# Optimization experiments

Measured on AMD Instinct MI355X. Metric: run time of the kernel, lower is better.

The kernel has to match this reference:

```python
import jax, jax.numpy as jnp
import numpy as np

B, CK, CQ, CV, CO, H, W = 4, 256, 256, 256, 64, 24, 24


def setup_inputs() -> dict:
    key = jax.random.key(0)
    ks = jax.random.split(key, 9)
    s = lambda k, shape, fan: jax.random.normal(k, shape, jnp.float32) * (fan ** -0.5)
    return {
        "key": jax.random.normal(ks[0], (B, CK, H, W), jnp.float32),
        "query": jax.random.normal(ks[1], (B, CQ, H, W), jnp.float32),
        "value": jax.random.normal(ks[2], (B, CV, H, W), jnp.float32),
        "Wk": s(ks[3], (CO, CK), CK),   # 1x1 conv weight for key transform
        "bk": jnp.zeros((CO,), jnp.float32),
        "Wq": s(ks[4], (CO, CQ), CQ),   # 1x1 conv weight for query transform
        "bq": jnp.zeros((CO,), jnp.float32),
        "wf": s(ks[5], (CO,), CO),      # channel-flattening 1x1 conv (CO -> 1)
        "bf": jnp.zeros((), jnp.float32),
    }


def reference(key, query, value, Wk, bk, Wq, bq, wf, bf):
    b, _, hq, wq = query.shape
    nk = key.shape[2] * key.shape[3]
    nq = hq * wq
    # 1x1 conv == per-pixel linear; flatten spatial to (B, N, CO)
    k_ = jnp.einsum('bchw,oc->bhwo', key, Wk).reshape(b, nk, -1) + bk
    q_ = jnp.einsum('bchw,oc->bhwo', query, Wq).reshape(b, nq, -1) + bq
    # broadcast add: (B, Nk, 1, CO) + (B, 1, Nq, CO) -> tanh -> reduce channels
    pre = jnp.tanh(k_[:, :, None, :] + q_[:, None, :, :])
    scores = jnp.einsum('bkqc,c->bkq', pre, wf) + bf
    attn = jax.nn.sigmoid(scores)                      # (B, Nk, Nq)
    v_ = value.reshape(b, value.shape[1], nk)          # (B, CV, Nk)
    out = jnp.einsum('bkq,bck->bcq', attn, v_)         # (B, CV, Nq)
    return out.reshape(b, value.shape[1], hq, wq)
```

## Files before the change

### kernel.cpp

```cpp
#include <hip/hip_runtime.h>
#include <hip/hip_bf16.h>

#define BB 4
#define CIN 256
#define CO 64
#define NN 576
#define NKC 18
#define NQT 36

typedef __attribute__((ext_vector_type(8))) short short8;
typedef __attribute__((ext_vector_type(4))) float floatx4;

__device__ __forceinline__ unsigned short f2bf(float f) {
    unsigned int u = __float_as_uint(f);
    unsigned int r = (u + 0x7fffu + ((u >> 16) & 1u)) >> 16;
    return (unsigned short)r;
}

__global__ void __launch_bounds__(256) prep_kernel(
    const float* __restrict__ key, const float* __restrict__ query,
    const float* __restrict__ value,
    const float* __restrict__ Wk, const float* __restrict__ Wq,
    const float* __restrict__ bk, const float* __restrict__ bq,
    float* __restrict__ ek, float* __restrict__ eq,
    unsigned short* __restrict__ Vp)
{
    __shared__ float red[4][4][64][4];
    __shared__ float ex[16 * 69];

    int bid = blockIdx.x;
    int t = threadIdx.x;
    int l = t & 63;
    int w = __builtin_amdgcn_readfirstlane(t >> 6);

    if (bid < 288) {
        int z  = bid / 144;
        int r  = bid % 144;
        int b  = r / 36;
        int nt = r % 36;
        int n0 = nt * 16;
        const float* x = z ? query : key;
        const float* W = z ? Wq : Wk;

        floatx4 acc[4] = {{0.f,0.f,0.f,0.f},{0.f,0.f,0.f,0.f},
                          {0.f,0.f,0.f,0.f},{0.f,0.f,0.f,0.f}};

        #pragma unroll
        for (int kci = 0; kci < 2; ++kci) {
            int kc = w + kci * 4;
            int cbase = kc * 32 + (l >> 4) * 8;
            const float* xp = x + ((size_t)b * CIN + cbase) * NN + n0 + (l & 15);
            uint4 bu;
            {
                float x0 = xp[0 * NN], x1 = xp[1 * NN], x2 = xp[2 * NN], x3 = xp[3 * NN];
                float x4 = xp[4 * NN], x5 = xp[5 * NN], x6 = xp[6 * NN], x7 = xp[7 * NN];
                bu.x = (unsigned)f2bf(x0) | ((unsigned)f2bf(x1) << 16);
                bu.y = (unsigned)f2bf(x2) | ((unsigned)f2bf(x3) << 16);
                bu.z = (unsigned)f2bf(x4) | ((unsigned)f2bf(x5) << 16);
                bu.w = (unsigned)f2bf(x6) | ((unsigned)f2bf(x7) << 16);
            }
            short8 bx = *(short8*)&bu;
            #pragma unroll
            for (int mt = 0; mt < 4; ++mt) {
                const float4* wp = (const float4*)(W + (size_t)(mt * 16 + (l & 15)) * CIN + cbase);
                float4 w0 = wp[0], w1 = wp[1];
                uint4 au;
                au.x = (unsigned)f2bf(w0.x) | ((unsigned)f2bf(w0.y) << 16);
                au.y = (unsigned)f2bf(w0.z) | ((unsigned)f2bf(w0.w) << 16);
                au.z = (unsigned)f2bf(w1.x) | ((unsigned)f2bf(w1.y) << 16);
                au.w = (unsigned)f2bf(w1.z) | ((unsigned)f2bf(w1.w) << 16);
                acc[mt] = __builtin_amdgcn_mfma_f32_16x16x32_bf16(*(short8*)&au, bx, acc[mt], 0, 0, 0);
            }
        }
        #pragma unroll
        for (int mt = 0; mt < 4; ++mt)
            #pragma unroll
            for (int rr = 0; rr < 4; ++rr)
                red[w][mt][l][rr] = acc[mt][rr];
        __syncthreads();

        const float* bias = z ? bq : bk;
        #pragma unroll
        for (int rr = 0; rr < 4; ++rr) {
            float v = red[0][w][l][rr] + red[1][w][l][rr]
                    + red[2][w][l][rr] + red[3][w][l][rr];
            int o = w * 16 + (l >> 4) * 4 + rr;
            ex[(l & 15) * 69 + o] = __expf(2.0f * (v + bias[o]));
        }
        __syncthreads();

        float* outp = z ? eq : ek;
        float* obase = outp + ((size_t)b * NN + n0) * CO;
        #pragma unroll
        for (int i = 0; i < 4; ++i) {
            int idx = t + i * 256;
            int n = idx >> 6, o = idx & 63;
            obase[(size_t)n * CO + o] = ex[n * 69 + o];
        }
    } else {
        int funit = (bid - 288) * 4 + w;
        int b  = funit / 288;
        int r2 = funit % 288;
        int ct = r2 / NKC;
        int kc = r2 % NKC;
        int c = ct * 16 + (l & 15);
        int k = kc * 32 + (l >> 4) * 8;
        const float4* p = (const float4*)(value + ((size_t)b * CIN + c) * NN + k);
        float4 v0 = p[0], v1 = p[1];
        uint4 u;
        u.x = (unsigned)f2bf(v0.x) | ((unsigned)f2bf(v0.y) << 16);
        u.y = (unsigned)f2bf(v0.z) | ((unsigned)f2bf(v0.w) << 16);
        u.z = (unsigned)f2bf(v1.x) | ((unsigned)f2bf(v1.y) << 16);
        u.w = (unsigned)f2bf(v1.z) | ((unsigned)f2bf(v1.w) << 16);
        *(uint4*)(Vp + (((size_t)b * 16 + ct) * NKC + kc) * 512 + l * 8) = u;
    }
}

__global__ void __launch_bounds__(256, 3) attn_pack_kernel(
    const float* __restrict__ ek, const float* __restrict__ eq,
    const float* __restrict__ wf, const float* __restrict__ bfp,
    unsigned short* __restrict__ Bp)
{
    int b  = blockIdx.z;
    int k0 = blockIdx.y * 32;
    int q0 = blockIdx.x * 64;
    int t  = threadIdx.x;
    int l  = t & 63;
    int w  = __builtin_amdgcn_readfirstlane(t >> 6);

    __shared__ float eqs[64 * 65];
    __shared__ float eks[32 * 68];
    __shared__ float w2s[64];
    __shared__ float Cs;
    __shared__ float sc[32 * 65];

    const float4* esrc = (const float4*)(eq + ((size_t)b * NN + q0) * CO);
    #pragma unroll
    for (int i = 0; i < 4; ++i) {
        int f4 = t + i * 256;
        int row = f4 >> 4, c4 = (f4 & 15) * 4;
        float4 v = esrc[f4];
        int a = row * 65 + c4;
        eqs[a] = v.x; eqs[a + 1] = v.y; eqs[a + 2] = v.z; eqs[a + 3] = v.w;
    }
    const float4* ksrc = (const float4*)(ek + ((size_t)b * NN + k0) * CO);
    #pragma unroll
    for (int i = 0; i < 2; ++i) {
        int f4 = t + i * 256;
        int row = f4 >> 4, c4 = (f4 & 15) * 4;
        *(float4*)&eks[row * 68 + c4] = ksrc[f4];
    }
    if (t < 64) {
        float v = wf[t];
        w2s[t] = 2.0f * v;
        #pragma unroll
        for (int s = 32; s; s >>= 1) v += __shfl_xor(v, s, 64);
        if (t == 0) Cs = v + bfp[0];
    }
    __syncthreads();

    float C = Cs;
    float4 eqv[16];
    #pragma unroll
    for (int i = 0; i < 16; ++i) {
        int a = l * 65 + i * 4;
        eqv[i].x = eqs[a]; eqv[i].y = eqs[a + 1];
        eqv[i].z = eqs[a + 2]; eqv[i].w = eqs[a + 3];
    }

    #pragma unroll 1
    for (int kk = 0; kk < 8; ++kk) {
        int krow = w * 8 + kk;
        const float* ekr = &eks[krow * 68];
        float a0 = 0.f, a1 = 0.f, a2 = 0.f, a3 = 0.f;
        #pragma unroll
        for (int i = 0; i < 16; ++i) {
            float4 k4 = *(const float4*)(ekr + i * 4);
            float4 w4 = *(const float4*)&w2s[i * 4];
            float4 e4 = eqv[i];
            a0 = fmaf(w4.x, __builtin_amdgcn_rcpf(fmaf(k4.x, e4.x, 1.0f)), a0);
            a1 = fmaf(w4.y, __builtin_amdgcn_rcpf(fmaf(k4.y, e4.y, 1.0f)), a1);
            a2 = fmaf(w4.z, __builtin_amdgcn_rcpf(fmaf(k4.z, e4.z, 1.0f)), a2);
            a3 = fmaf(w4.w, __builtin_amdgcn_rcpf(fmaf(k4.w, e4.w, 1.0f)), a3);
        }
        float score = C - (a0 + a1) - (a2 + a3);
        float sg = __builtin_amdgcn_rcpf(1.0f + __expf(-score));
        sc[krow * 65 + l] = sg;
    }
    __syncthreads();

    int col = w * 16 + (l & 15);
    int row = (l >> 4) * 8;
    uint4 o;
    o.x = (unsigned)f2bf(sc[(row + 0) * 65 + col]) | ((unsigned)f2bf(sc[(row + 1) * 65 + col]) << 16);
    o.y = (unsigned)f2bf(sc[(row + 2) * 65 + col]) | ((unsigned)f2bf(sc[(row + 3) * 65 + col]) << 16);
    o.z = (unsigned)f2bf(sc[(row + 4) * 65 + col]) | ((unsigned)f2bf(sc[(row + 5) * 65 + col]) << 16);
    o.w = (unsigned)f2bf(sc[(row + 6) * 65 + col]) | ((unsigned)f2bf(sc[(row + 7) * 65 + col]) << 16);
    size_t qt = (size_t)blockIdx.x * 4 + w;
    *(uint4*)(Bp + (((size_t)b * NQT + qt) * NKC + blockIdx.y) * 512 + l * 8) = o;
}

__global__ void __launch_bounds__(256) av_mfma_kernel(
    const unsigned short* __restrict__ Vp,
    const unsigned short* __restrict__ Bp,
    float* __restrict__ out)
{
    int b  = blockIdx.z;
    int ct = blockIdx.y;
    int qx = blockIdx.x;
    int t  = threadIdx.x;
    int l  = t & 63;
    int w  = __builtin_amdgcn_readfirstlane(t >> 6);

    floatx4 acc[4] = {{0.f,0.f,0.f,0.f},{0.f,0.f,0.f,0.f},
                      {0.f,0.f,0.f,0.f},{0.f,0.f,0.f,0.f}};

    const unsigned short* abase = Vp + ((size_t)b * 16 + ct) * NKC * 512 + l * 8;
    const unsigned short* bbase = Bp + ((size_t)b * NQT + (size_t)qx * 4) * NKC * 512 + l * 8;

    for (int kc = w; kc < NKC; kc += 4) {
        short8 a = *(const short8*)(abase + (size_t)kc * 512);
        #pragma unroll
        for (int qt = 0; qt < 4; ++qt) {
            short8 bq = *(const short8*)(bbase + ((size_t)qt * NKC + kc) * 512);
            acc[qt] = __builtin_amdgcn_mfma_f32_16x16x32_bf16(a, bq, acc[qt], 0, 0, 0);
        }
    }

    __shared__ float red[4][64][17];
    #pragma unroll
    for (int qt = 0; qt < 4; ++qt)
        #pragma unroll
        for (int r = 0; r < 4; ++r)
            red[w][l][qt * 4 + r] = acc[qt][r];
    __syncthreads();

    int q = qx * 64 + w * 16 + (l & 15);
    #pragma unroll
    for (int r = 0; r < 4; ++r) {
        float s = red[0][l][w * 4 + r] + red[1][l][w * 4 + r]
                + red[2][l][w * 4 + r] + red[3][l][w * 4 + r];
        int c = ct * 16 + (l >> 4) * 4 + r;
        out[((size_t)b * CIN + c) * NN + q] = s;
    }
}

extern "C" void kernel_launch(void* const* d_in, const int* in_sizes, int n_in,
                              void* d_out, int out_size, void* d_ws, size_t ws_size,
                              hipStream_t stream) {
    const float* key   = (const float*)d_in[0];
    const float* query = (const float*)d_in[1];
    const float* value = (const float*)d_in[2];
    const float* Wk    = (const float*)d_in[3];
    const float* bk    = (const float*)d_in[4];
    const float* Wq    = (const float*)d_in[5];
    const float* bq    = (const float*)d_in[6];
    const float* wf    = (const float*)d_in[7];
    const float* bf    = (const float*)d_in[8];
    float* out = (float*)d_out;

    float* ws = (float*)d_ws;
    float* ek = ws;
    float* eq = ek + (size_t)BB * NN * CO;
    unsigned short* Vp = (unsigned short*)(eq + (size_t)BB * NN * CO);
    unsigned short* Bp = Vp + (size_t)BB * 16 * NKC * 512;

    prep_kernel<<<576, 256, 0, stream>>>(key, query, value, Wk, Wq, bk, bq, ek, eq, Vp);

    dim3 ga(NN / 64, NN / 32, BB);
    attn_pack_kernel<<<ga, 256, 0, stream>>>(ek, eq, wf, bf, Bp);

    dim3 gm(NN / 64, 16, BB);
    av_mfma_kernel<<<gm, 256, 0, stream>>>(Vp, Bp, out);
}
```

Baseline: 108.1 us.

## Stage input tile in LDS for coalesced loads and fold tanh scale into ek

The projection stage now loads each 256x16 input tile with coalesced float4 reads, transposes it into shared memory, and swaps the MFMA operand roles so the output tile is stored row-contiguous. This replaces the strided per-element global reads of the old path. It also folds the factor 2 on wf into ek by scaling ek by 0.5 and using a 0.5 constant in the reciprocal. That saves a multiply per weight load, and the tanh identity stays mathematically the same. The cost is extra LDS (about 16KB more) and an additional barrier.

```diff
diff --git a/kernel.cpp b/kernel.cpp
--- a/kernel.cpp
+++ b/kernel.cpp
@@ -6,6 +6,7 @@
 #define CO 64
 #define NN 576
 #define NKC 18
+#define NMT 36
 #define NQT 36
 
 typedef __attribute__((ext_vector_type(8))) short short8;
@@ -25,8 +26,9 @@
     float* __restrict__ ek, float* __restrict__ eq,
     unsigned short* __restrict__ Vp)
 {
+    __shared__ float xs[16 * 260];
     __shared__ float red[4][4][64][4];
-    __shared__ float ex[16 * 69];
+    __shared__ float ex[16 * 68];
 
     int bid = blockIdx.x;
     int t = threadIdx.x;
@@ -36,66 +38,77 @@
     if (bid < 288) {
         int z  = bid / 144;
         int r  = bid % 144;
-        int b  = r / 36;
-        int nt = r % 36;
-        int n0 = nt * 16;
+        int b  = r / NMT;
+        int mt = r % NMT;
+        int n0 = mt * 16;
         const float* x = z ? query : key;
         const float* W = z ? Wq : Wk;
 
+        const float* xbase = x + (size_t)b * CIN * NN + n0;
+        #pragma unroll
+        for (int i = 0; i < 4; ++i) {
+            int f4 = t + i * 256;
+            int c = f4 >> 2, nl4 = (f4 & 3) * 4;
+            float4 v = *(const float4*)(xbase + (size_t)c * NN + nl4);
+            xs[(nl4 + 0) * 260 + c] = v.x;
+            xs[(nl4 + 1) * 260 + c] = v.y;
+            xs[(nl4 + 2) * 260 + c] = v.z;
+            xs[(nl4 + 3) * 260 + c] = v.w;
+        }
+        __syncthreads();
+
         floatx4 acc[4] = {{0.f,0.f,0.f,0.f},{0.f,0.f,0.f,0.f},
                           {0.f,0.f,0.f,0.f},{0.f,0.f,0.f,0.f}};
-
         #pragma unroll
         for (int kci = 0; kci < 2; ++kci) {
-            int kc = w + kci * 4;
-            int cbase = kc * 32 + (l >> 4) * 8;
-            const float* xp = x + ((size_t)b * CIN + cbase) * NN + n0 + (l & 15);
-            uint4 bu;
-            {
-                float x0 = xp[0 * NN], x1 = xp[1 * NN], x2 = xp[2 * NN], x3 = xp[3 * NN];
-                float x4 = xp[4 * NN], x5 = xp[5 * NN], x6 = xp[6 * NN], x7 = xp[7 * NN];
-                bu.x = (unsigned)f2bf(x0) | ((unsigned)f2bf(x1) << 16);
-                bu.y = (unsigned)f2bf(x2) | ((unsigned)f2bf(x3) << 16);
-                bu.z = (unsigned)f2bf(x4) | ((unsigned)f2bf(x5) << 16);
-                bu.w = (unsigned)f2bf(x6) | ((unsigned)f2bf(x7) << 16);
+            int kc = w * 2 + kci;
+            int c0 = kc * 32 + (l >> 4) * 8;
+            float4 xa = *(const float4*)&xs[(l & 15) * 260 + c0];
+            float4 xb = *(const float4*)&xs[(l & 15) * 260 + c0 + 4];
+            uint4 au;
+            au.x = (unsigned)f2bf(xa.x) | ((unsigned)f2bf(xa.y) << 16);
+            au.y = (unsigned)f2bf(xa.z) | ((unsigned)f2bf(xa.w) << 16);
+            au.z = (unsigned)f2bf(xb.x) | ((unsigned)f2bf(xb.y) << 16);
+            au.w = (unsigned)f2bf(xb.z) | ((unsigned)f2bf(xb.w) << 16);
+            short8 xf = *(short8*)&au;
+            #pragma unroll
+            for (int nt = 0; nt < 4; ++nt) {
+                const float4* wp = (const float4*)(W + (size_t)(nt * 16 + (l & 15)) * CIN + c0);
+                float4 w0 = wp[0], w1 = wp[1];
+                uint4 bu;
+                bu.x = (unsigned)f2bf(w0.x) | ((unsigned)f2bf(w0.y) << 16);
+                bu.y = (unsigned)f2bf(w0.z) | ((unsigned)f2bf(w0.w) << 16);
+                bu.z = (unsigned)f2bf(w1.x) | ((unsigned)f2bf(w1.y) << 16);
+                bu.w = (unsigned)f2bf(w1.z) | ((unsigned)f2bf(w1.w) << 16);
+                acc[nt] = __builtin_amdgcn_mfma_f32_16x16x32_bf16(xf, *(short8*)&bu, acc[nt], 0, 0, 0);
             }
-            short8 bx = *(short8*)&bu;
-            #pragma unroll
-            for (int mt = 0; mt < 4; ++mt) {
-                const float4* wp = (const float4*)(W + (size_t)(mt * 16 + (l & 15)) * CIN + cbase);
-                float4 w0 = wp[0], w1 = wp[1];
-                uint4 au;
-                au.x = (unsigned)f2bf(w0.x) | ((unsigned)f2bf(w0.y) << 16);
-                au.y = (unsigned)f2bf(w0.z) | ((unsigned)f2bf(w0.w) << 16);
-                au.z = (unsigned)f2bf(w1.x) | ((unsigned)f2bf(w1.y) << 16);
-                au.w = (unsigned)f2bf(w1.z) | ((unsigned)f2bf(w1.w) << 16);
-                acc[mt] = __builtin_amdgcn_mfma_f32_16x16x32_bf16(*(short8*)&au, bx, acc[mt], 0, 0, 0);
-            }
-        }
-        #pragma unroll
-        for (int mt = 0; mt < 4; ++mt)
+        }
+        #pragma unroll
+        for (int nt = 0; nt < 4; ++nt)
             #pragma unroll
             for (int rr = 0; rr < 4; ++rr)
-                red[w][mt][l][rr] = acc[mt][rr];
+                red[w][nt][l][rr] = acc[nt][rr];
         __syncthreads();
 
         const float* bias = z ? bq : bk;
+        float scale = z ? 1.0f : 0.5f;
         #pragma unroll
         for (int rr = 0; rr < 4; ++rr) {
             float v = red[0][w][l][rr] + red[1][w][l][rr]
                     + red[2][w][l][rr] + red[3][w][l][rr];
-            int o = w * 16 + (l >> 4) * 4 + rr;
-            ex[(l & 15) * 69 + o] = __expf(2.0f * (v + bias[o]));
+            int o = w * 16 + (l & 15);
+            int n = (l >> 4) * 4 + rr;
+            ex[n * 68 + o] = scale * __expf(2.0f * (v + bias[o]));
         }
         __syncthreads();
 
-        float* outp = z ? eq : ek;
+        float* outp  = z ? eq : ek;
         float* obase = outp + ((size_t)b * NN + n0) * CO;
         #pragma unroll
         for (int i = 0; i < 4; ++i) {
             int idx = t + i * 256;
             int n = idx >> 6, o = idx & 63;
-            obase[(size_t)n * CO + o] = ex[n * 69 + o];
+            obase[idx] = ex[n * 68 + o];
         }
     } else {
         int funit = (bid - 288) * 4 + w;
@@ -152,7 +165,7 @@
     }
     if (t < 64) {
         float v = wf[t];
-        w2s[t] = 2.0f * v;
+        w2s[t] = v;
         #pragma unroll
         for (int s = 32; s; s >>= 1) v += __shfl_xor(v, s, 64);
         if (t == 0) Cs = v + bfp[0];
@@ -178,10 +191,10 @@
             float4 k4 = *(const float4*)(ekr + i * 4);
             float4 w4 = *(const float4*)&w2s[i * 4];
             float4 e4 = eqv[i];
-            a0 = fmaf(w4.x, __builtin_amdgcn_rcpf(fmaf(k4.x, e4.x, 1.0f)), a0);
-            a1 = fmaf(w4.y, __builtin_amdgcn_rcpf(fmaf(k4.y, e4.y, 1.0f)), a1);
-            a2 = fmaf(w4.z, __builtin_amdgcn_rcpf(fmaf(k4.z, e4.z, 1.0f)), a2);
-            a3 = fmaf(w4.w, __builtin_amdgcn_rcpf(fmaf(k4.w, e4.w, 1.0f)), a3);
+            a0 = fmaf(w4.x, __builtin_amdgcn_rcpf(fmaf(k4.x, e4.x, 0.5f)), a0);
+            a1 = fmaf(w4.y, __builtin_amdgcn_rcpf(fmaf(k4.y, e4.y, 0.5f)), a1);
+            a2 = fmaf(w4.z, __builtin_amdgcn_rcpf(fmaf(k4.z, e4.z, 0.5f)), a2);
+            a3 = fmaf(w4.w, __builtin_amdgcn_rcpf(fmaf(k4.w, e4.w, 0.5f)), a3);
         }
         float score = C - (a0 + a1) - (a2 + a3);
         float sg = __builtin_amdgcn_rcpf(1.0f + __expf(-score));
```

New measurement: 110.0 us. Within noise of the previous version (+1.7%).
